# Kernel tuning notes

Hardware: AMD Instinct MI355X
Metric: run time of the kernel (lower is better)

## Reference

```python
import jax, jax.numpy as jnp
import numpy as np

N_LINKS = 100000
N_EDGES = 1600000
D = 64          # link_state_dim
RU = 256        # readout_units
G = 256         # number of graphs
T = 4           # message passing iterations


def _glorot(key, shape):
    fan_in, fan_out = shape[0], shape[1]
    limit = np.sqrt(6.0 / (fan_in + fan_out)).astype(np.float32)
    return jax.random.uniform(key, shape, jnp.float32, -limit, limit)


def setup_inputs() -> dict:
    key = jax.random.key(0)
    ks = jax.random.split(key, 12)
    states_action = jax.random.normal(ks[0], (N_LINKS, D), jnp.float32)
    states_graph_ids = jnp.sort(jax.random.randint(ks[1], (N_LINKS,), 0, G))
    states_first = jax.random.randint(ks[2], (N_EDGES,), 0, N_LINKS)
    states_second = jax.random.randint(ks[3], (N_EDGES,), 0, N_LINKS)
    # Message: Dense(2D -> D) with selu
    W_msg = _glorot(ks[4], (2 * D, D)); b_msg = jnp.zeros((D,), jnp.float32)
    # GCN: Linear(D -> D) + relu, then unsorted_segment_sum
    W_gcn = _glorot(ks[5], (D, D)); b_gcn = jnp.zeros((D,), jnp.float32)
    # Readout MLP: D -> RU -> RU -> 1
    W_r1 = _glorot(ks[6], (D, RU)); b_r1 = jnp.zeros((RU,), jnp.float32)
    W_r2 = _glorot(ks[7], (RU, RU)); b_r2 = jnp.zeros((RU,), jnp.float32)
    W_r3 = _glorot(ks[8], (RU, 1)); b_r3 = jnp.zeros((1,), jnp.float32)
    return {
        "states_action": states_action,
        "W_msg": W_msg, "b_msg": b_msg,
        "W_gcn": W_gcn, "b_gcn": b_gcn,
        "W_r1": W_r1, "b_r1": b_r1,
        "W_r2": W_r2, "b_r2": b_r2,
        "W_r3": W_r3, "b_r3": b_r3,
        "states_graph_ids": states_graph_ids,
        "states_first": states_first,
        "states_second": states_second,
        "sates_num_edges": N_EDGES,
    }


def reference(states_action, W_msg, b_msg, W_gcn, b_gcn,
              W_r1, b_r1, W_r2, b_r2, W_r3, b_r3,
              states_graph_ids, states_first, states_second, sates_num_edges):
    n_links = states_action.shape[0]
    link_state = states_action
    for _ in range(T):
        main_e = link_state[states_first]      # [E, D]
        neigh_e = link_state[states_second]    # [E, D]
        concat = jnp.concatenate([main_e, neigh_e], axis=1)  # [E, 2D]
        msg = jax.nn.selu(concat @ W_msg + b_msg)            # [E, D]
        h = jax.nn.relu(msg @ W_gcn + b_gcn)                 # [E, D]
        # scatter-add messages back onto links (segment ids = states_second)
        link_state = jax.ops.segment_sum(h, states_second, num_segments=n_links)
        # dropout rate is 0.0 -> identity
    # per-graph readout (graph ids are sorted, fixed G segments)
    graph_emb = jax.ops.segment_sum(link_state, states_graph_ids, num_segments=G)
    r = jax.nn.selu(graph_emb @ W_r1 + b_r1)
    r = jax.nn.selu(r @ W_r2 + b_r2)
    r = r @ W_r3 + b_r3                                      # [G, 1]
    return r
```

## Files before the change

kernel.cpp:

```cpp
#include <hip/hip_runtime.h>
#include <hip/hip_bf16.h>
#include <math.h>

#define D 64
#define RU 256
#define CHUNK 8
#define QSTRIDE 68
#define BIN_SHIFT 7
#define NSB 128

#if __has_builtin(__builtin_amdgcn_exp2f)
#define EXP2F(x) __builtin_amdgcn_exp2f(x)
#else
#define EXP2F(x) exp2f(x)
#endif

typedef short bf16x8 __attribute__((ext_vector_type(8)));
typedef float f32x4 __attribute__((ext_vector_type(4)));

__device__ __forceinline__ float selu_f(float x) {
    return x > 0.0f ? 1.0507009873554805f * x
                    : 1.7580993408473766f * (__expf(x) - 1.0f);
}

__device__ __forceinline__ float selu_x2(float x2) {
    const float p = fmaxf(x2, 0.0f);
    const float n = fminf(x2, 0.0f);
    const float e = EXP2F(n);
    return fmaf(1.7580993408473766f, e, fmaf(0.72829042516f, p, -1.7580993408473766f));
}

__device__ __forceinline__ short f2bf_rtne(float x) {
    union { float f; unsigned u; } v; v.f = x;
    unsigned r = (v.u + 0x7FFFu + ((v.u >> 16) & 1u)) >> 16;
    return (short)r;
}
__device__ __forceinline__ float bf2f(short s) {
    union { float f; unsigned u; } v; v.u = ((unsigned)(unsigned short)s) << 16;
    return v.f;
}
__device__ __forceinline__ unsigned packpair(float a, float b) {
    float2 p; p.x = a; p.y = b;
    __hip_bfloat162 hb = __float22bfloat162_rn(p);
    return *(unsigned*)&hb;
}

__device__ __forceinline__ bf16x8 pack8(const float* v) {
    union { bf16x8 v; unsigned u[4]; } H;
#pragma unroll
    for (int j = 0; j < 4; ++j) H.u[j] = packpair(v[2 * j], v[2 * j + 1]);
    return H.v;
}

#define FIDX(ks, jt, qd, m) ((((((ks) * 4 + (jt)) * 4 + (qd)) * 16) + (m)) * 8)

__global__ __launch_bounds__(256) void wprep_kernel(
    const float* __restrict__ W_msg, const float* __restrict__ W_gcn,
    const float* __restrict__ b_gcn,
    unsigned short* __restrict__ WAh, unsigned short* __restrict__ WAl,
    unsigned short* __restrict__ WBh, unsigned short* __restrict__ WBl,
    unsigned short* __restrict__ WGh, float* __restrict__ cstar,
    unsigned short* __restrict__ Pb, int n_links)
{
    const float LOG2E = 1.4426950408889634f;
    const int t = blockIdx.x * 256 + threadIdx.x;

    if (blockIdx.x == 0 && threadIdx.x < 64) {
        const int col = threadIdx.x;
        Pb[(size_t)n_links * 64 + col] = 0xFF80;
        const float c0 = bf2f(f2bf_rtne(-1.7580993408473766f));
        float acc = b_gcn[col];
        for (int k = 0; k < 64; ++k)
            acc = fmaf(c0, bf2f(f2bf_rtne(W_gcn[k * 64 + col])), acc);
        cstar[col] = fmaxf(acc, 0.0f);
    }

    if (t >= 4096) return;
    const int i  = t & 7;
    const int m  = (t >> 3) & 15;
    const int qd = (t >> 7) & 3;
    const int jt = (t >> 9) & 3;
    const int ks = t >> 11;
    const int kk = ks * 32 + qd * 8 + i;
    const int nn = jt * 16 + m;

    float w = W_msg[kk * 64 + nn] * LOG2E;
    short hi = f2bf_rtne(w);
    WAh[t] = (unsigned short)hi;
    WAl[t] = (unsigned short)f2bf_rtne(w - bf2f(hi));

    w = W_msg[(64 + kk) * 64 + nn] * LOG2E;
    hi = f2bf_rtne(w);
    WBh[t] = (unsigned short)hi;
    WBl[t] = (unsigned short)f2bf_rtne(w - bf2f(hi));

    WGh[t] = (unsigned short)f2bf_rtne(W_gcn[kk * 64 + nn]);
}

__global__ __launch_bounds__(256) void s2bf_kernel(
    const float* __restrict__ in, unsigned short* __restrict__ out, int n4)
{
    for (int i = blockIdx.x * 256 + threadIdx.x; i < n4; i += gridDim.x * 256) {
        const float4 v = ((const float4*)in)[i];
        uint2 o;
        o.x = packpair(v.x, v.y);
        o.y = packpair(v.z, v.w);
        ((uint2*)out)[i] = o;
    }
}


__global__ __launch_bounds__(256) void histA_kernel(
    const int* __restrict__ second, int* __restrict__ ghist,
    int n_edges, int nbins)
{
    __shared__ int lhist[1024];
    for (int i = threadIdx.x; i < nbins; i += 256) lhist[i] = 0;
    __syncthreads();
    const int per = (n_edges + gridDim.x - 1) / gridDim.x;
    const int e0 = blockIdx.x * per;
    const int e1 = min(e0 + per, n_edges);
    for (int e = e0 + threadIdx.x; e < e1; e += 256)
        atomicAdd(&lhist[second[e] >> BIN_SHIFT], 1);
    __syncthreads();
    for (int i = threadIdx.x; i < nbins; i += 256)
        ghist[i * gridDim.x + blockIdx.x] = lhist[i];
}

__global__ __launch_bounds__(64) void sumbins_kernel(
    int* __restrict__ ghist, int* __restrict__ btot, int nbins)
{
    const int b = blockIdx.x, tid = threadIdx.x;
    const int d0 = ghist[b * NSB + tid];
    const int d1 = ghist[b * NSB + 64 + tid];
    int p0 = d0, p1 = d1;
#pragma unroll
    for (int off = 1; off < 64; off <<= 1) {
        const int t0 = __shfl_up(p0, off, 64);
        const int t1 = __shfl_up(p1, off, 64);
        if (tid >= off) { p0 += t0; p1 += t1; }
    }
    const int tot0 = __shfl(p0, 63, 64);
    ghist[b * NSB + tid] = p0 - d0;
    ghist[b * NSB + 64 + tid] = tot0 + p1 - d1;
    if (tid == 63) btot[b] = tot0 + p1;
}

__global__ __launch_bounds__(1024) void scanS_kernel(int* __restrict__ data, int n)
{
    __shared__ int wsum[16], woff[16];
    const int tid = threadIdx.x, wave = tid >> 6, lane = tid & 63;
    const int x = (tid < n) ? data[tid] : 0;
    int v = x;
#pragma unroll
    for (int off = 1; off < 64; off <<= 1) {
        const int t = __shfl_up(v, off, 64);
        if (lane >= off) v += t;
    }
    if (lane == 63) wsum[wave] = v;
    __syncthreads();
    if (wave == 0) {
        int s = (lane < 16) ? wsum[lane] : 0;
#pragma unroll
        for (int off = 1; off < 16; off <<= 1) {
            const int t = __shfl_up(s, off, 64);
            if (lane >= off) s += t;
        }
        if (lane < 16) woff[lane] = s - wsum[lane];
    }
    __syncthreads();
    if (tid < n) data[tid] = woff[wave] + v - x;
}

__global__ __launch_bounds__(256) void scatterC_kernel(
    const int* __restrict__ first, const int* __restrict__ second,
    const int* __restrict__ ghist, const int* __restrict__ btot,
    unsigned* __restrict__ tmp, int n_edges, int nbins)
{
    __shared__ int lcur[1024];
    for (int i = threadIdx.x; i < nbins; i += 256)
        lcur[i] = ghist[i * NSB + blockIdx.x] + btot[i];
    __syncthreads();
    const int per = (n_edges + gridDim.x - 1) / gridDim.x;
    const int e0 = blockIdx.x * per;
    const int e1 = min(e0 + per, n_edges);
    for (int e = e0 + threadIdx.x; e < e1; e += 256) {
        const int s = second[e];
        const int pos = atomicAdd(&lcur[s >> BIN_SHIFT], 1);
        tmp[pos] = (unsigned)first[e] | ((unsigned)(s & 127) << 20);
    }
}

__global__ __launch_bounds__(256) void binsortD_kernel(
    const unsigned* __restrict__ tmp, const int* __restrict__ btot,
    int* __restrict__ sfirst, int* __restrict__ row_ptr, int* __restrict__ ptot,
    int n_edges, int n_links, int nbins)
{
    __shared__ int ldeg[128];
    __shared__ int lpre[128];
    __shared__ int lcur[128];
    const int b = blockIdx.x;
    const int tid = threadIdx.x;
    const int lbase = b << BIN_SHIFT;
    const int nl = min(128, n_links - lbase);
    const int eb = btot[b];
    const int ee = (b + 1 < nbins) ? btot[b + 1] : n_edges;

    if (tid < 128) ldeg[tid] = 0;
    __syncthreads();
    for (int e = eb + tid; e < ee; e += 256)
        atomicAdd(&ldeg[tmp[e] >> 20], 1);
    __syncthreads();
    if (tid < 64) {
        const int d0 = ldeg[tid], d1 = ldeg[64 + tid];
        int p0 = d0, p1 = d1;
#pragma unroll
        for (int off = 1; off < 64; off <<= 1) {
            const int t0 = __shfl_up(p0, off, 64);
            const int t1 = __shfl_up(p1, off, 64);
            if (tid >= off) { p0 += t0; p1 += t1; }
        }
        const int tot0 = __shfl(p0, 63, 64);
        lpre[tid] = p0 - d0;
        lpre[64 + tid] = tot0 + p1 - d1;
        const int n0 = (d0 + 15) >> 4, n1 = (d1 + 15) >> 4;
        int q0 = n0, q1 = n1;
#pragma unroll
        for (int off = 1; off < 64; off <<= 1) {
            const int t0 = __shfl_up(q0, off, 64);
            const int t1 = __shfl_up(q1, off, 64);
            if (tid >= off) { q0 += t0; q1 += t1; }
        }
        if (tid == 63) ptot[b] = q0 + q1;
    }
    __syncthreads();
    if (tid < nl) row_ptr[lbase + tid] = eb + lpre[tid];
    if (b == nbins - 1 && tid == 0) row_ptr[n_links] = n_edges;
    if (tid < 128) lcur[tid] = lpre[tid];
    __syncthreads();
    for (int e = eb + tid; e < ee; e += 256) {
        const unsigned v = tmp[e];
        const int pos = eb + atomicAdd(&lcur[v >> 20], 1);
        sfirst[pos] = (int)(v & 0xFFFFFu);
    }
    if (b == 0)
        for (int i = tid; i < 64; i += 256) sfirst[n_edges + i] = 0;
}

__global__ __launch_bounds__(256) void tbuild_kernel(
    const int* __restrict__ row_ptr, const int* __restrict__ tbase,
    int* __restrict__ ptile, int* __restrict__ tinfo,
    int n_links, int nbins)
{
    __shared__ int rpl[130];
    __shared__ int ltp[130];
    const int b = blockIdx.x, tid = threadIdx.x;
    const int lbase = b << BIN_SHIFT;
    const int nl = min(128, n_links - lbase);
    if (tid <= nl) rpl[tid] = row_ptr[lbase + tid];
    __syncthreads();
    if (tid < 64) {
        const int d0 = (tid < nl) ? rpl[tid + 1] - rpl[tid] : 0;
        const int d1 = (64 + tid < nl) ? rpl[64 + tid + 1] - rpl[64 + tid] : 0;
        const int n0 = (d0 + 15) >> 4, n1 = (d1 + 15) >> 4;
        int p0 = n0, p1 = n1;
#pragma unroll
        for (int off = 1; off < 64; off <<= 1) {
            const int t0 = __shfl_up(p0, off, 64);
            const int t1 = __shfl_up(p1, off, 64);
            if (tid >= off) { p0 += t0; p1 += t1; }
        }
        const int tot0 = __shfl(p0, 63, 64);
        ltp[tid] = p0 - n0;
        ltp[64 + tid] = tot0 + p1 - n1;
        if (tid == 63) ltp[128] = tot0 + p1;
    }
    __syncthreads();
    const int tb = tbase[b];
    if (tid <= nl) ptile[lbase + tid] = tb + ltp[tid];
    const int ntb = ltp[128];
    for (int tl = tid; tl < ntb; tl += 256) {
        int lo = 0, hi = nl - 1;
        while (lo < hi) {
            const int mid = (lo + hi + 1) >> 1;
            if (ltp[mid] <= tl) lo = mid; else hi = mid - 1;
        }
        const int li = lo;
        const int eo = rpl[li] + ((tl - ltp[li]) << 4);
        const int rend = rpl[li + 1];
        const int vc = min(16, rend - eo);
        const int last = (eo + 16 >= rend) ? 1 : 0;
        tinfo[tb + tl] = eo | ((li & 7) << 21) | (last << 24) | (vc << 25);
    }
    if (b == nbins - 1 && tid < 8) tinfo[tb + ntb + tid] = 0;
}

__global__ __launch_bounds__(256) void growfind_kernel(
    const int* __restrict__ gid, int* __restrict__ grow, int n_links, int G)
{
    const int g = blockIdx.x * blockDim.x + threadIdx.x;
    if (g > G) return;
    if (g == G) { grow[G] = n_links; return; }
    int lo = 0, hi = n_links;
    while (lo < hi) {
        const int mid = (lo + hi) >> 1;
        if (gid[mid] < g) lo = mid + 1; else hi = mid;
    }
    grow[g] = lo;
}

__global__ __launch_bounds__(256) void p_mfma_kernel(
    const unsigned short* __restrict__ Sb,
    const unsigned short* __restrict__ WAh, const unsigned short* __restrict__ WAl,
    unsigned short* __restrict__ P, int n_links)
{
    const int tid = threadIdx.x;
    const int wave = tid >> 6;
    const int lane = tid & 63;
    const int m = lane & 15;
    const int qd = lane >> 4;

    bf16x8 Bh[2][4], Bl[2][4];
#pragma unroll
    for (int ks = 0; ks < 2; ++ks)
#pragma unroll
        for (int jt = 0; jt < 4; ++jt) {
            const int off = FIDX(ks, jt, qd, m);
            Bh[ks][jt] = *(const bf16x8*)(WAh + off);
            Bl[ks][jt] = *(const bf16x8*)(WAl + off);
        }
    const bf16x8 z = (bf16x8){0, 0, 0, 0, 0, 0, 0, 0};

    const int ngroups = (n_links + 63) >> 6;
    for (int g = blockIdx.x; g < ngroups; g += gridDim.x) {
        const int base = g * 64 + wave * 16;
        const int l = base + m;
        bf16x8 Ah0 = z, Ah1 = z;
        if (l < n_links) {
            Ah0 = *(const bf16x8*)(Sb + (size_t)l * D + qd * 8);
            Ah1 = *(const bf16x8*)(Sb + (size_t)l * D + 32 + qd * 8);
        }
        f32x4 accP[4];
#pragma unroll
        for (int jt = 0; jt < 4; ++jt) {
            accP[jt] = (f32x4){0.f, 0.f, 0.f, 0.f};
            accP[jt] = __builtin_amdgcn_mfma_f32_16x16x32_bf16(Ah0, Bh[0][jt], accP[jt], 0, 0, 0);
            accP[jt] = __builtin_amdgcn_mfma_f32_16x16x32_bf16(Ah0, Bl[0][jt], accP[jt], 0, 0, 0);
            accP[jt] = __builtin_amdgcn_mfma_f32_16x16x32_bf16(Ah1, Bh[1][jt], accP[jt], 0, 0, 0);
            accP[jt] = __builtin_amdgcn_mfma_f32_16x16x32_bf16(Ah1, Bl[1][jt], accP[jt], 0, 0, 0);
        }
#pragma unroll
        for (int r = 0; r < 4; ++r) {
            const int lr = base + qd * 4 + r;
            if (lr < n_links) {
#pragma unroll
                for (int jt = 0; jt < 4; ++jt)
                    P[(size_t)lr * D + jt * 16 + m] =
                        (unsigned short)f2bf_rtne(accP[jt][r]);
            }
        }
    }
}

__global__ __launch_bounds__(256, 4) void edge_link_kernel(
    unsigned short* __restrict__ Sb, const unsigned short* __restrict__ P,
    const int* __restrict__ sfirst, const int* __restrict__ tinfo,
    const int* __restrict__ ptile,
    const float* __restrict__ b_msg,
    const unsigned short* __restrict__ WBh, const unsigned short* __restrict__ WBl,
    const unsigned short* __restrict__ WGh,
    const float* __restrict__ b_gcn, const float* __restrict__ cstar,
    int n_links)
{
    __shared__ float qt[4][CHUNK * QSTRIDE + 4];
    __shared__ float cbl[64];
    const int tid = threadIdx.x;
    const int wave = tid >> 6;
    const int lane = tid & 63;
    const int m = lane & 15;
    const int qd = lane >> 4;

    cbl[lane] = cstar[lane];

    const int l0 = (blockIdx.x * 4 + wave) * CHUNK;
    if (l0 >= n_links) return;
    const int nl = min(CHUNK, n_links - l0);

    const float LOG2E = 1.4426950408889634f;
    float bmsgC[4];
#pragma unroll
    for (int jt = 0; jt < 4; ++jt) bmsgC[jt] = b_msg[jt * 16 + m] * LOG2E;

    {
        const bf16x8 z = (bf16x8){0, 0, 0, 0, 0, 0, 0, 0};
        const int l = l0 + m;
        bf16x8 Ah0 = z, Ah1 = z;
        if ((l < n_links) && (m < CHUNK)) {
            Ah0 = *(const bf16x8*)(Sb + (size_t)l * D + qd * 8);
            Ah1 = *(const bf16x8*)(Sb + (size_t)l * D + 32 + qd * 8);
        }
        f32x4 accQ[4];
#pragma unroll
        for (int jt = 0; jt < 4; ++jt) accQ[jt] = (f32x4){0.f, 0.f, 0.f, 0.f};
#pragma unroll
        for (int ks = 0; ks < 2; ++ks) {
            bf16x8 WbH[4], WbL[4];
#pragma unroll
            for (int jt = 0; jt < 4; ++jt) {
                const int off = FIDX(ks, jt, qd, m);
                WbH[jt] = *(const bf16x8*)(WBh + off);
                WbL[jt] = *(const bf16x8*)(WBl + off);
            }
            const bf16x8 A = ks ? Ah1 : Ah0;
#pragma unroll
            for (int jt = 0; jt < 4; ++jt) {
                accQ[jt] = __builtin_amdgcn_mfma_f32_16x16x32_bf16(A, WbH[jt], accQ[jt], 0, 0, 0);
                accQ[jt] = __builtin_amdgcn_mfma_f32_16x16x32_bf16(A, WbL[jt], accQ[jt], 0, 0, 0);
            }
        }
#pragma unroll
        for (int r = 0; r < 4; ++r) {
            const int row = qd * 4 + r;
            if (row < CHUNK) {
#pragma unroll
                for (int jt = 0; jt < 4; ++jt)
                    qt[wave][row * QSTRIDE + jt * 16 + m] = accQ[jt][r] + bmsgC[jt];
            }
        }
    }

    bf16x8 Gh[2][4];
#pragma unroll
    for (int ks = 0; ks < 2; ++ks)
#pragma unroll
        for (int jt = 0; jt < 4; ++jt)
            Gh[ks][jt] = *(const bf16x8*)(WGh + FIDX(ks, jt, qd, m));

    float bias_gcn[4];
#pragma unroll
    for (int jt = 0; jt < 4; ++jt) bias_gcn[jt] = b_gcn[jt * 16 + m];

    const int tpv = ptile[l0 + min(lane, nl)];
#pragma unroll
    for (int i = 0; i < CHUNK; ++i) {
        if (i < nl && __shfl(tpv, i + 1, 64) == __shfl(tpv, i, 64))
            Sb[(size_t)(l0 + i) * D + lane] = 0;
    }
    const int tbeg = __builtin_amdgcn_readfirstlane(tpv);
    const int tend = __builtin_amdgcn_readfirstlane(__shfl(tpv, nl, 64));
    if (tbeg >= tend) return;

    int ti0 = tinfo[tbeg];
    int ti1 = tinfo[tbeg + 1];
    int ti2 = tinfo[tbeg + 2];

    bf16x8 p00, p01;
    {
        const int eo = ti0 & 0x1FFFFF, vc = (ti0 >> 25) & 31;
        int sf = sfirst[eo + m];
        sf = (m < vc) ? sf : n_links;
        const unsigned short* Pr = P + (size_t)sf * D;
        p00 = *(const bf16x8*)(Pr + qd * 8);
        p01 = *(const bf16x8*)(Pr + 32 + qd * 8);
    }
    int sf1;
    {
        const int eo = ti1 & 0x1FFFFF, vc = (ti1 >> 25) & 31;
        int sf = sfirst[eo + m];
        sf1 = (m < vc) ? sf : n_links;
    }

    float rsum[4] = {0.f, 0.f, 0.f, 0.f};

    for (int t = tbeg; t < tend; ++t) {
        const int tiN = tinfo[t + 3];
        const int eo2 = ti2 & 0x1FFFFF, vc2 = (ti2 >> 25) & 31;
        int sf2 = sfirst[eo2 + m];
        sf2 = (m < vc2) ? sf2 : n_links;
        const unsigned short* Pr1 = P + (size_t)sf1 * D;
        const bf16x8 p10 = *(const bf16x8*)(Pr1 + qd * 8);
        const bf16x8 p11 = *(const bf16x8*)(Pr1 + 32 + qd * 8);

        const int li0 = (ti0 >> 21) & 7;
        const int vc0 = (ti0 >> 25) & 31;
        const int qoff = li0 * QSTRIDE + qd * 8;

        float msgA[8];
        {
            const float4 qa0 = *(const float4*)&qt[wave][qoff];
            const float4 qa1 = *(const float4*)&qt[wave][qoff + 4];
#pragma unroll
            for (int i = 0; i < 4; ++i) {
                msgA[i]     = selu_x2(bf2f(p00[i])     + qa0[i]);
                msgA[4 + i] = selu_x2(bf2f(p00[4 + i]) + qa1[i]);
            }
        }
        const bf16x8 Ah0 = pack8(msgA);
        float msgB[8];
        {
            const float4 qb0 = *(const float4*)&qt[wave][qoff + 32];
            const float4 qb1 = *(const float4*)&qt[wave][qoff + 36];
#pragma unroll
            for (int i = 0; i < 4; ++i) {
                msgB[i]     = selu_x2(bf2f(p01[i])     + qb0[i]);
                msgB[4 + i] = selu_x2(bf2f(p01[4 + i]) + qb1[i]);
            }
        }
        const bf16x8 Ah1 = pack8(msgB);

        f32x4 acc[4];
#pragma unroll
        for (int jt = 0; jt < 4; ++jt) {
            const float b = bias_gcn[jt];
            acc[jt] = (f32x4){b, b, b, b};
            acc[jt] = __builtin_amdgcn_mfma_f32_16x16x32_bf16(Ah0, Gh[0][jt], acc[jt], 0, 0, 0);
            acc[jt] = __builtin_amdgcn_mfma_f32_16x16x32_bf16(Ah1, Gh[1][jt], acc[jt], 0, 0, 0);
        }
#pragma unroll
        for (int jt = 0; jt < 4; ++jt)
#pragma unroll
            for (int r = 0; r < 4; ++r)
                rsum[jt] += fmaxf(acc[jt][r], 0.0f);

        if (ti0 & (1 << 24)) {
            const int over = qd * 4 + 4 - vc0;
            const float cnt = (float)max(0, min(4, over));
#pragma unroll
            for (int jt = 0; jt < 4; ++jt) {
                rsum[jt] -= cbl[jt * 16 + m] * cnt;
                rsum[jt] += __shfl_xor(rsum[jt], 16, 64);
                rsum[jt] += __shfl_xor(rsum[jt], 32, 64);
            }
            const float outv = (qd == 0) ? rsum[0] : (qd == 1) ? rsum[1]
                             : (qd == 2) ? rsum[2] : rsum[3];
            Sb[(size_t)(l0 + li0) * D + lane] = (unsigned short)f2bf_rtne(outv);
#pragma unroll
            for (int jt = 0; jt < 4; ++jt) rsum[jt] = 0.0f;
        }

        ti0 = ti1; ti1 = ti2; ti2 = tiN;
        sf1 = sf2;
        p00 = p10; p01 = p11;
    }
}

__global__ __launch_bounds__(256) void gsum8_kernel(
    const unsigned short* __restrict__ Sb, const int* __restrict__ grow,
    float* __restrict__ gemb)
{
    __shared__ float red[4][64];
    const int g = blockIdx.x >> 3;
    const int slice = blockIdx.x & 7;
    const int slot = threadIdx.x >> 6;
    const int j = threadIdx.x & 63;
    const int ls = grow[g], le = grow[g + 1];
    float acc = 0.0f;
    for (int l = ls + slice * 4 + slot; l < le; l += 32)
        acc += bf2f((short)Sb[(size_t)l * D + j]);
    red[slot][j] = acc;
    __syncthreads();
    if (slot == 0)
        atomicAdd(&gemb[g * D + j], red[0][j] + red[1][j] + red[2][j] + red[3][j]);
}

__global__ __launch_bounds__(256) void mlp_kernel(
    const float* __restrict__ gemb,
    const float* __restrict__ W_r1, const float* __restrict__ b_r1,
    const float* __restrict__ W_r2, const float* __restrict__ b_r2,
    const float* __restrict__ W_r3, const float* __restrict__ b_r3,
    float* __restrict__ out)
{
    __shared__ float gl[64];
    __shared__ float row1[RU];
    __shared__ float row2[RU];
    __shared__ float fin[4];
    const int g = blockIdx.x;
    const int tid = threadIdx.x;
    const int slot = tid >> 6;
    const int lane = tid & 63;

    if (tid < 64) gl[tid] = gemb[g * D + tid];
    __syncthreads();

    float a1 = b_r1[tid];
#pragma unroll 8
    for (int k = 0; k < 64; ++k) a1 += gl[k] * W_r1[k * RU + tid];
    row1[tid] = selu_f(a1);
    __syncthreads();

    float a2 = b_r2[tid];
#pragma unroll 8
    for (int k = 0; k < RU; ++k) a2 += row1[k] * W_r2[k * RU + tid];
    row2[tid] = selu_f(a2);
    __syncthreads();

    float p = row2[tid] * W_r3[tid];
#pragma unroll
    for (int off = 32; off >= 1; off >>= 1)
        p += __shfl_down(p, off, 64);
    if (lane == 0) fin[slot] = p;
    __syncthreads();
    if (tid == 0)
        out[g] = fin[0] + fin[1] + fin[2] + fin[3] + b_r3[0];
}

extern "C" void kernel_launch(void* const* d_in, const int* in_sizes, int n_in,
                              void* d_out, int out_size, void* d_ws, size_t ws_size,
                              hipStream_t stream)
{
    const float* states_action = (const float*)d_in[0];
    const float* W_msg = (const float*)d_in[1];
    const float* b_msg = (const float*)d_in[2];
    const float* W_gcn = (const float*)d_in[3];
    const float* b_gcn = (const float*)d_in[4];
    const float* W_r1 = (const float*)d_in[5];
    const float* b_r1 = (const float*)d_in[6];
    const float* W_r2 = (const float*)d_in[7];
    const float* b_r2 = (const float*)d_in[8];
    const float* W_r3 = (const float*)d_in[9];
    const float* b_r3 = (const float*)d_in[10];
    const int* gid = (const int*)d_in[11];
    const int* first = (const int*)d_in[12];
    const int* second = (const int*)d_in[13];

    const int n_links = in_sizes[0] / D;
    const int n_edges = in_sizes[12];
    const int G = out_size;
    const int nbins = (n_links + 127) >> BIN_SHIFT;

    char* ws2 = (char*)d_ws;
    auto alloc = [&](size_t bytes) {
        char* p = ws2; ws2 += (bytes + 63) & ~(size_t)63; return p;
    };
    unsigned short* Sb = (unsigned short*)alloc((size_t)n_links * D * 2);
    unsigned short* Pb = (unsigned short*)alloc((size_t)(n_links + 1) * D * 2);
    float* gemb = (float*)alloc((size_t)G * D * sizeof(float));
    int* row_ptr = (int*)alloc((size_t)(n_links + 1) * sizeof(int));
    int* grow = (int*)alloc((size_t)(G + 1) * sizeof(int));
    int* ghist = (int*)alloc((size_t)nbins * NSB * sizeof(int));
    unsigned* tmp = (unsigned*)alloc((size_t)n_edges * sizeof(unsigned));
    int* sfirst = (int*)alloc((size_t)(n_edges + 64) * sizeof(int));
    unsigned short* WAh = (unsigned short*)alloc(4096 * 2);
    unsigned short* WAl = (unsigned short*)alloc(4096 * 2);
    unsigned short* WBh = (unsigned short*)alloc(4096 * 2);
    unsigned short* WBl = (unsigned short*)alloc(4096 * 2);
    unsigned short* WGh = (unsigned short*)alloc(4096 * 2);
    int* btot = (int*)alloc((size_t)nbins * sizeof(int));
    int* ptotv = (int*)alloc((size_t)nbins * sizeof(int));
    int* ptile = (int*)alloc((size_t)(n_links + 1) * sizeof(int));
    float* cstar = (float*)alloc(64 * sizeof(float));
    int* tinfoA = (int*)tmp;

    hipMemsetAsync(gemb, 0, (size_t)G * D * sizeof(float), stream);
    s2bf_kernel<<<1024, 256, 0, stream>>>(states_action, Sb, n_links * D / 4);
    wprep_kernel<<<16, 256, 0, stream>>>(W_msg, W_gcn, b_gcn, WAh, WAl, WBh, WBl,
                                         WGh, cstar, Pb, n_links);
    histA_kernel<<<NSB, 256, 0, stream>>>(second, ghist, n_edges, nbins);
    sumbins_kernel<<<nbins, 64, 0, stream>>>(ghist, btot, nbins);
    scanS_kernel<<<1, 1024, 0, stream>>>(btot, nbins);
    scatterC_kernel<<<NSB, 256, 0, stream>>>(first, second, ghist, btot, tmp,
                                             n_edges, nbins);
    binsortD_kernel<<<nbins, 256, 0, stream>>>(tmp, btot, sfirst, row_ptr, ptotv,
                                               n_edges, n_links, nbins);
    scanS_kernel<<<1, 1024, 0, stream>>>(ptotv, nbins);
    tbuild_kernel<<<nbins, 256, 0, stream>>>(row_ptr, ptotv, ptile, tinfoA,
                                             n_links, nbins);
    growfind_kernel<<<2, 256, 0, stream>>>(gid, grow, n_links, G);

    const int edge_blocks = (n_links + 4 * CHUNK - 1) / (4 * CHUNK);
    for (int t = 0; t < 4; ++t) {
        p_mfma_kernel<<<782, 256, 0, stream>>>(Sb, WAh, WAl, Pb, n_links);
        edge_link_kernel<<<edge_blocks, 256, 0, stream>>>(Sb, Pb, sfirst, tinfoA,
                                                          ptile, b_msg, WBh, WBl,
                                                          WGh, b_gcn, cstar,
                                                          n_links);
    }

    gsum8_kernel<<<G * 8, 256, 0, stream>>>(Sb, grow, gemb);
    mlp_kernel<<<G, 256, 0, stream>>>(gemb, W_r1, b_r1, W_r2, b_r2,
                                      W_r3, b_r3, (float*)d_out);
}
```

Baseline: 528.2 us.

## Widen histogram sub-blocks, cache q-vector in registers, enlarge p_mfma grid

Raises the number of histogram sub-blocks from 128 to 256 and generalises the bin prefix sum to four segments per bin. The histogram buffer now aliases the sfirst workspace instead of taking its own allocation. The edge kernel keeps the per-link q values in registers and reloads them from shared memory only when the local link index changes, saving LDS reads per tile. The p_mfma launch grows from 782 to 1024 blocks. Aliasing ghist onto sfirst relies on sfirst not being written until after the scatter step finishes reading ghist.

```diff
diff --git a/kernel.cpp b/kernel.cpp
--- a/kernel.cpp
+++ b/kernel.cpp
@@ -7,7 +7,7 @@
 #define CHUNK 8
 #define QSTRIDE 68
 #define BIN_SHIFT 7
-#define NSB 128
+#define NSB 256
 
 #if __has_builtin(__builtin_amdgcn_exp2f)
 #define EXP2F(x) __builtin_amdgcn_exp2f(x)
@@ -131,19 +131,28 @@
     int* __restrict__ ghist, int* __restrict__ btot, int nbins)
 {
     const int b = blockIdx.x, tid = threadIdx.x;
-    const int d0 = ghist[b * NSB + tid];
-    const int d1 = ghist[b * NSB + 64 + tid];
-    int p0 = d0, p1 = d1;
+    int d[4], p[4];
+#pragma unroll
+    for (int k = 0; k < 4; ++k) {
+        d[k] = ghist[b * NSB + k * 64 + tid];
+        p[k] = d[k];
+    }
 #pragma unroll
     for (int off = 1; off < 64; off <<= 1) {
-        const int t0 = __shfl_up(p0, off, 64);
-        const int t1 = __shfl_up(p1, off, 64);
-        if (tid >= off) { p0 += t0; p1 += t1; }
-    }
-    const int tot0 = __shfl(p0, 63, 64);
-    ghist[b * NSB + tid] = p0 - d0;
-    ghist[b * NSB + 64 + tid] = tot0 + p1 - d1;
-    if (tid == 63) btot[b] = tot0 + p1;
+#pragma unroll
+        for (int k = 0; k < 4; ++k) {
+            const int t = __shfl_up(p[k], off, 64);
+            if (tid >= off) p[k] += t;
+        }
+    }
+    int base = 0;
+#pragma unroll
+    for (int k = 0; k < 4; ++k) {
+        const int tot = __shfl(p[k], 63, 64);
+        ghist[b * NSB + k * 64 + tid] = base + p[k] - d[k];
+        base += tot;
+    }
+    if (tid == 63) btot[b] = base;
 }
 
 __global__ __launch_bounds__(1024) void scanS_kernel(int* __restrict__ data, int n)
@@ -470,6 +479,8 @@
         sf1 = (m < vc) ? sf : n_links;
     }
 
+    float qb[16];
+    int qli = -1;
     float rsum[4] = {0.f, 0.f, 0.f, 0.f};
 
     for (int t = tbeg; t < tend; ++t) {
@@ -483,29 +494,25 @@
 
         const int li0 = (ti0 >> 21) & 7;
         const int vc0 = (ti0 >> 25) & 31;
-        const int qoff = li0 * QSTRIDE + qd * 8;
+
+        if (li0 != qli) {
+            qli = li0;
+            const int qoff = li0 * QSTRIDE + qd * 8;
+            *(float4*)&qb[0]  = *(const float4*)&qt[wave][qoff];
+            *(float4*)&qb[4]  = *(const float4*)&qt[wave][qoff + 4];
+            *(float4*)&qb[8]  = *(const float4*)&qt[wave][qoff + 32];
+            *(float4*)&qb[12] = *(const float4*)&qt[wave][qoff + 36];
+        }
 
         float msgA[8];
-        {
-            const float4 qa0 = *(const float4*)&qt[wave][qoff];
-            const float4 qa1 = *(const float4*)&qt[wave][qoff + 4];
-#pragma unroll
-            for (int i = 0; i < 4; ++i) {
-                msgA[i]     = selu_x2(bf2f(p00[i])     + qa0[i]);
-                msgA[4 + i] = selu_x2(bf2f(p00[4 + i]) + qa1[i]);
-            }
-        }
+#pragma unroll
+        for (int i = 0; i < 8; ++i)
+            msgA[i] = selu_x2(bf2f(p00[i]) + qb[i]);
         const bf16x8 Ah0 = pack8(msgA);
         float msgB[8];
-        {
-            const float4 qb0 = *(const float4*)&qt[wave][qoff + 32];
-            const float4 qb1 = *(const float4*)&qt[wave][qoff + 36];
-#pragma unroll
-            for (int i = 0; i < 4; ++i) {
-                msgB[i]     = selu_x2(bf2f(p01[i])     + qb0[i]);
-                msgB[4 + i] = selu_x2(bf2f(p01[4 + i]) + qb1[i]);
-            }
-        }
+#pragma unroll
+        for (int i = 0; i < 8; ++i)
+            msgB[i] = selu_x2(bf2f(p01[i]) + qb[8 + i]);
         const bf16x8 Ah1 = pack8(msgB);
 
         f32x4 acc[4];
@@ -637,7 +644,6 @@
     float* gemb = (float*)alloc((size_t)G * D * sizeof(float));
     int* row_ptr = (int*)alloc((size_t)(n_links + 1) * sizeof(int));
     int* grow = (int*)alloc((size_t)(G + 1) * sizeof(int));
-    int* ghist = (int*)alloc((size_t)nbins * NSB * sizeof(int));
     unsigned* tmp = (unsigned*)alloc((size_t)n_edges * sizeof(unsigned));
     int* sfirst = (int*)alloc((size_t)(n_edges + 64) * sizeof(int));
     unsigned short* WAh = (unsigned short*)alloc(4096 * 2);
@@ -650,6 +656,7 @@
     int* ptile = (int*)alloc((size_t)(n_links + 1) * sizeof(int));
     float* cstar = (float*)alloc(64 * sizeof(float));
     int* tinfoA = (int*)tmp;
+    int* ghist = (int*)sfirst;
 
     hipMemsetAsync(gemb, 0, (size_t)G * D * sizeof(float), stream);
     s2bf_kernel<<<1024, 256, 0, stream>>>(states_action, Sb, n_links * D / 4);
@@ -669,7 +676,7 @@
 
     const int edge_blocks = (n_links + 4 * CHUNK - 1) / (4 * CHUNK);
     for (int t = 0; t < 4; ++t) {
-        p_mfma_kernel<<<782, 256, 0, stream>>>(Sb, WAh, WAl, Pb, n_links);
+        p_mfma_kernel<<<1024, 256, 0, stream>>>(Sb, WAh, WAl, Pb, n_links);
         edge_link_kernel<<<edge_blocks, 256, 0, stream>>>(Sb, Pb, sfirst, tinfoA,
                                                           ptile, b_msg, WBh, WBl,
                                                           WGh, b_gcn, cstar,
```

Measured after the change: 521.8 us. About the same (-1.2%).
